# Optimization experiments

Measured on AMD Instinct MI355X. Metric: run time of the kernel, lower is better.

## Reference

```python
import jax, jax.numpy as jnp
import numpy as np

N, E, D = 100000, 1600000, 128      # nodes, edges, in_channels = MLP out_dim
L = 3                               # num GIN layers
OC = D + L * D                      # concat width = 512
CH, CHID = 4, 256                   # num ChannelMLPs, their hidden dim


def setup_inputs() -> dict:
    key = jax.random.key(0)
    ks = jax.random.split(key, 10)
    s = lambda fan_in: 1.0 / np.sqrt(fan_in)
    x = jax.random.normal(ks[0], (N, D), dtype=jnp.float32)
    edge_index = jax.random.randint(ks[1], (2, E), 0, N, dtype=jnp.int32)
    # conv MLPs: per layer 3 linear layers (in->hid, hid->hid, hid->out), all 128x128
    convW = jax.random.normal(ks[2], (L, 3, D, D), dtype=jnp.float32) * s(D)
    convB = jnp.zeros((L, 3, D), dtype=jnp.float32)
    # channel MLPs: 512 -> 256 -> 256 -> 1, ReLU after every layer (output_activation='relu')
    chanW1 = jax.random.normal(ks[3], (CH, OC, CHID), dtype=jnp.float32) * s(OC)
    chanB1 = jnp.zeros((CH, CHID), dtype=jnp.float32)
    chanW2 = jax.random.normal(ks[4], (CH, CHID, CHID), dtype=jnp.float32) * s(CHID)
    chanB2 = jnp.zeros((CH, CHID), dtype=jnp.float32)
    chanW3 = jax.random.normal(ks[5], (CH, CHID, 1), dtype=jnp.float32) * s(CHID)
    chanB3 = jnp.zeros((CH, 1), dtype=jnp.float32)
    return {"x": x, "edge_index": edge_index, "convW": convW, "convB": convB,
            "chanW1": chanW1, "chanB1": chanB1, "chanW2": chanW2, "chanB2": chanB2,
            "chanW3": chanW3, "chanB3": chanB3}


def reference(x, edge_index, convW, convB, chanW1, chanB1, chanW2, chanB2, chanW3, chanB3):
    src, dst = edge_index[0], edge_index[1]
    n = x.shape[0]
    feats = [x]                      # skip_first_features=False -> keep input
    h = x
    for l in range(L):
        # GINConv, eps=0: mlp((1+eps)*h + sum_{j in N(i)} h_j)
        agg = jax.ops.segment_sum(h[src], dst, num_segments=n)  # scatter-add at targets
        h = h + agg
        for k in range(3):           # MLP: Lin+ReLU x3 (2 hidden + relu output activation)
            h = jax.nn.relu(h @ convW[l, k] + convB[l, k])
        feats.append(h)
    xcat = jnp.concatenate(feats, axis=1)                       # [N, 512]
    # channel MLPs vectorized over the channel axis c
    h1 = jax.nn.relu(jnp.einsum('nd,cdh->cnh', xcat, chanW1) + chanB1[:, None, :])
    h2 = jax.nn.relu(jnp.einsum('cnh,chk->cnk', h1, chanW2) + chanB2[:, None, :])
    h3 = jax.nn.relu(jnp.einsum('cnh,cho->cno', h2, chanW3) + chanB3[:, None, :])
    return jnp.transpose(h3[..., 0])                            # [N, num_ChannelMLPs]
```

## Files before the change

kernel.cpp:

```cpp
#include <hip/hip_runtime.h>
#include <hip/hip_bf16.h>

#define D 128
#define NLAYER 3
#define NCH 4

typedef __attribute__((ext_vector_type(8))) short short8;
typedef __attribute__((ext_vector_type(4))) float f32x4;

__device__ __forceinline__ ushort f2bf(float f) {
    unsigned int u = __builtin_bit_cast(unsigned int, f);
    u += 0x7fffu + ((u >> 16) & 1u);
    return (ushort)(u >> 16);
}
__device__ __forceinline__ float bflo(unsigned int u) {
    return __builtin_bit_cast(float, u << 16);
}
__device__ __forceinline__ float bfhi(unsigned int u) {
    return __builtin_bit_cast(float, u & 0xffff0000u);
}

#define FILL_CHUNK 4096
__global__ __launch_bounds__(256) void hist_part_kernel(
    const int* __restrict__ dst, int* __restrict__ deg,
    int E, int nPer, int N)
{
    int cls = blockIdx.x & 7;
    int base = (blockIdx.x >> 3) * FILL_CHUNK;
    int lo = cls * nPer;
    int hi = lo + nPer; if (hi > N) hi = N;
    int end = base + FILL_CHUNK; if (end > E) end = E;
    for (int e = base + threadIdx.x; e < end; e += 256) {
        int d = dst[e];
        if (d >= lo && d < hi) atomicAdd(&deg[d], 1);
    }
}

__global__ __launch_bounds__(256) void blocksum_kernel(
    const int* __restrict__ deg, int* __restrict__ bsum, int n)
{
    int i = blockIdx.x * 256 + threadIdx.x;
    int v = (i < n) ? deg[i] : 0;
#pragma unroll
    for (int o = 1; o < 64; o <<= 1) v += __shfl_xor(v, o);
    __shared__ int s[4];
    if ((threadIdx.x & 63) == 0) s[threadIdx.x >> 6] = v;
    __syncthreads();
    if (threadIdx.x == 0) bsum[blockIdx.x] = s[0] + s[1] + s[2] + s[3];
}

__global__ __launch_bounds__(512) void scanblk_kernel(
    const int* __restrict__ bsum, int* __restrict__ boff, int nb,
    int* __restrict__ offs, int n, int E)
{
    __shared__ int sh[512];
    int t = threadIdx.x;
    sh[t] = (t < nb) ? bsum[t] : 0;
    __syncthreads();
    for (int d = 1; d < 512; d <<= 1) {
        int v = (t >= d) ? sh[t - d] : 0;
        __syncthreads();
        sh[t] += v;
        __syncthreads();
    }
    if (t < nb) boff[t] = (t == 0) ? 0 : sh[t - 1];
    if (t == 0) offs[n] = E;
}

__global__ __launch_bounds__(256) void blockscan_kernel(
    const int* __restrict__ deg, const int* __restrict__ boff,
    int* __restrict__ offs, int* __restrict__ cursor, int n)
{
    __shared__ int sh[256];
    int t = threadIdx.x;
    int i = blockIdx.x * 256 + t;
    int v = (i < n) ? deg[i] : 0;
    sh[t] = v;
    __syncthreads();
    for (int d = 1; d < 256; d <<= 1) {
        int u = (t >= d) ? sh[t - d] : 0;
        __syncthreads();
        sh[t] += u;
        __syncthreads();
    }
    if (i < n) {
        int ex = boff[blockIdx.x] + sh[t] - v;
        offs[i] = ex; cursor[i] = ex;
    }
}

__global__ __launch_bounds__(256) void fill_part_kernel(
    const int* __restrict__ src, const int* __restrict__ dst,
    int* __restrict__ cursor, int* __restrict__ csr,
    int E, int nPer, int N)
{
    int cls = blockIdx.x & 7;
    int base = (blockIdx.x >> 3) * FILL_CHUNK;
    int lo = cls * nPer;
    int hi = lo + nPer; if (hi > N) hi = N;
    int end = base + FILL_CHUNK; if (end > E) end = E;
    for (int e = base + threadIdx.x; e < end; e += 256) {
        int d = dst[e];
        int s = src[e];
        if (d >= lo && d < hi) {
            int p = atomicAdd(&cursor[d], 1);
            csr[p] = s;
        }
    }
}

__global__ __launch_bounds__(256) void cvtx_kernel(
    const float* __restrict__ x, ushort* __restrict__ xb, int total8)
{
    int i = blockIdx.x * 256 + threadIdx.x;
    if (i >= total8) return;
    const float* gp = x + (size_t)i * 8;
    float4 v0 = *(const float4*)gp;
    float4 v1 = *(const float4*)(gp + 4);
    short8 pk;
    pk[0] = (short)f2bf(v0.x); pk[1] = (short)f2bf(v0.y);
    pk[2] = (short)f2bf(v0.z); pk[3] = (short)f2bf(v0.w);
    pk[4] = (short)f2bf(v1.x); pk[5] = (short)f2bf(v1.y);
    pk[6] = (short)f2bf(v1.z); pk[7] = (short)f2bf(v1.w);
    *(short8*)(xb + (size_t)i * 8) = pk;
}

__global__ void cvtW_kernel(const float* __restrict__ W, ushort* __restrict__ Wt,
                            int K, int Ncols) {
    __shared__ float tile[32][33];
    int c = blockIdx.z;
    int k0 = blockIdx.x * 32, n0 = blockIdx.y * 32;
    const float* Wc = W + (size_t)c * K * Ncols;
    ushort* Wtc = Wt + (size_t)c * K * Ncols;
    int tx = threadIdx.x & 31, ty = threadIdx.x >> 5;
#pragma unroll
    for (int i = 0; i < 4; ++i) {
        int k = k0 + ty + i * 8;
        tile[ty + i * 8][tx] = Wc[(size_t)k * Ncols + n0 + tx];
    }
    __syncthreads();
#pragma unroll
    for (int i = 0; i < 4; ++i) {
        int n = n0 + ty + i * 8;
        Wtc[(size_t)n * K + k0 + tx] = f2bf(tile[tx][ty + i * 8]);
    }
}

__global__ __launch_bounds__(256) void agg_bf16(
    const ushort* __restrict__ h,
    const int* __restrict__ offs, const int* __restrict__ csr,
    ushort* __restrict__ outb, int n)
{
    int node = (blockIdx.x * 256 + threadIdx.x) >> 4;
    int l16 = threadIdx.x & 15;
    if (node >= n) return;
    uint4 u = *((const uint4*)(h + (size_t)node * 128) + l16);
    float a0 = bflo(u.x), a1 = bfhi(u.x);
    float a2 = bflo(u.y), a3 = bfhi(u.y);
    float a4 = bflo(u.z), a5 = bfhi(u.z);
    float a6 = bflo(u.w), a7 = bfhi(u.w);
    int b = offs[node], e = offs[node + 1];
    int j = b;
    for (; j + 4 <= e; j += 4) {
        int s0 = csr[j], s1 = csr[j + 1], s2 = csr[j + 2], s3 = csr[j + 3];
        uint4 v0 = *((const uint4*)(h + (size_t)s0 * 128) + l16);
        uint4 v1 = *((const uint4*)(h + (size_t)s1 * 128) + l16);
        uint4 v2 = *((const uint4*)(h + (size_t)s2 * 128) + l16);
        uint4 v3 = *((const uint4*)(h + (size_t)s3 * 128) + l16);
        a0 += (bflo(v0.x) + bflo(v1.x)) + (bflo(v2.x) + bflo(v3.x));
        a1 += (bfhi(v0.x) + bfhi(v1.x)) + (bfhi(v2.x) + bfhi(v3.x));
        a2 += (bflo(v0.y) + bflo(v1.y)) + (bflo(v2.y) + bflo(v3.y));
        a3 += (bfhi(v0.y) + bfhi(v1.y)) + (bfhi(v2.y) + bfhi(v3.y));
        a4 += (bflo(v0.z) + bflo(v1.z)) + (bflo(v2.z) + bflo(v3.z));
        a5 += (bfhi(v0.z) + bfhi(v1.z)) + (bfhi(v2.z) + bfhi(v3.z));
        a6 += (bflo(v0.w) + bflo(v1.w)) + (bflo(v2.w) + bflo(v3.w));
        a7 += (bfhi(v0.w) + bfhi(v1.w)) + (bfhi(v2.w) + bfhi(v3.w));
    }
    for (; j < e; ++j) {
        uint4 v0 = *((const uint4*)(h + (size_t)csr[j] * 128) + l16);
        a0 += bflo(v0.x); a1 += bfhi(v0.x);
        a2 += bflo(v0.y); a3 += bfhi(v0.y);
        a4 += bflo(v0.z); a5 += bfhi(v0.z);
        a6 += bflo(v0.w); a7 += bfhi(v0.w);
    }
    uint4 po;
    po.x = (unsigned int)f2bf(a0) | ((unsigned int)f2bf(a1) << 16);
    po.y = (unsigned int)f2bf(a2) | ((unsigned int)f2bf(a3) << 16);
    po.z = (unsigned int)f2bf(a4) | ((unsigned int)f2bf(a5) << 16);
    po.w = (unsigned int)f2bf(a6) | ((unsigned int)f2bf(a7) << 16);
    *((uint4*)(outb + (size_t)node * 128) + l16) = po;
}

__global__ __launch_bounds__(256) void gin_mlp_mfma(
    const ushort* __restrict__ A,
    const ushort* __restrict__ WtL,
    const float* __restrict__ biasL,
    ushort* __restrict__ Out,
    int nrows)
{
    __shared__ __align__(16) ushort As[128 * 128];
    __shared__ __align__(16) ushort Bs[128 * 128];
    const int t = threadIdx.x;
    const int w = t >> 6, lane = t & 63;
    const int quad = lane >> 4, c15 = lane & 15;
    const int wr = w >> 1, wc = w & 1;
    const int rowbase = blockIdx.x * 128;

#pragma unroll
    for (int i = 0; i < 8; ++i) {
        int lin = (i * 4 + w) * 64 + lane;
        int row = lin >> 4, slot = lin & 15, g = slot ^ (row & 15);
        int grow = rowbase + row;
        if (grow >= nrows) grow = 0;
        const ushort* gp = A + (size_t)grow * 128 + g * 8;
        __builtin_amdgcn_global_load_lds(
            (const __attribute__((address_space(1))) void*)gp,
            (__attribute__((address_space(3))) void*)&As[(i * 4 + w) * 512],
            16, 0, 0);
    }
#pragma unroll
    for (int i = 0; i < 8; ++i) {
        int lin = (i * 4 + w) * 64 + lane;
        int n = lin >> 4, slot = lin & 15, g = slot ^ (n & 15);
        const ushort* gp = WtL + (size_t)n * 128 + g * 8;
        __builtin_amdgcn_global_load_lds(
            (const __attribute__((address_space(1))) void*)gp,
            (__attribute__((address_space(3))) void*)&Bs[(i * 4 + w) * 512],
            16, 0, 0);
    }
    __syncthreads();

    for (int s = 0; s < 3; ++s) {
        f32x4 acc[4][4];
#pragma unroll
        for (int i = 0; i < 4; ++i)
#pragma unroll
            for (int j = 0; j < 4; ++j)
#pragma unroll
                for (int r = 0; r < 4; ++r) acc[i][j][r] = 0.f;

#pragma unroll
        for (int ks = 0; ks < 4; ++ks) {
            short8 af[4], bf[4];
#pragma unroll
            for (int tr = 0; tr < 4; ++tr) {
                int r = wr * 64 + tr * 16 + c15;
                af[tr] = *(const short8*)&As[r * 128 + (((ks * 4 + quad) ^ (r & 15)) * 8)];
            }
#pragma unroll
            for (int tc = 0; tc < 4; ++tc) {
                int n = wc * 64 + tc * 16 + c15;
                bf[tc] = *(const short8*)&Bs[n * 128 + (((ks * 4 + quad) ^ (n & 15)) * 8)];
            }
#pragma unroll
            for (int tr = 0; tr < 4; ++tr)
#pragma unroll
                for (int tc = 0; tc < 4; ++tc)
                    acc[tr][tc] = __builtin_amdgcn_mfma_f32_16x16x32_bf16(
                        af[tr], bf[tc], acc[tr][tc], 0, 0, 0);
        }
        __syncthreads();

        if (s < 2) {
#pragma unroll
            for (int tc = 0; tc < 4; ++tc) {
                int col = wc * 64 + tc * 16 + c15;
                float bv = biasL[s * 128 + col];
#pragma unroll
                for (int tr = 0; tr < 4; ++tr)
#pragma unroll
                    for (int rg = 0; rg < 4; ++rg) {
                        int row = wr * 64 + tr * 16 + quad * 4 + rg;
                        As[row * 128 + (((col >> 3) ^ (row & 15)) * 8) + (col & 7)]
                            = f2bf(fmaxf(acc[tr][tc][rg] + bv, 0.f));
                    }
            }
            const ushort* Wn = WtL + (size_t)(s + 1) * 128 * 128;
#pragma unroll
            for (int i = 0; i < 8; ++i) {
                int lin = (i * 4 + w) * 64 + lane;
                int n = lin >> 4, slot = lin & 15, g = slot ^ (n & 15);
                const ushort* gp = Wn + (size_t)n * 128 + g * 8;
                __builtin_amdgcn_global_load_lds(
                    (const __attribute__((address_space(1))) void*)gp,
                    (__attribute__((address_space(3))) void*)&Bs[(i * 4 + w) * 512],
                    16, 0, 0);
            }
            __syncthreads();
        } else {
#pragma unroll
            for (int tc = 0; tc < 4; ++tc) {
                int col = wc * 64 + tc * 16 + c15;
                float bv = biasL[2 * 128 + col];
#pragma unroll
                for (int tr = 0; tr < 4; ++tr)
#pragma unroll
                    for (int rg = 0; rg < 4; ++rg) {
                        int grow = rowbase + wr * 64 + tr * 16 + quad * 4 + rg;
                        if (grow < nrows)
                            Out[(size_t)grow * 128 + col]
                                = f2bf(fmaxf(acc[tr][tc][rg] + bv, 0.f));
                    }
            }
        }
    }
}

__global__ __launch_bounds__(256, 2) void chan_fused_mfma(
    const ushort* __restrict__ A0, const ushort* __restrict__ A1,
    const ushort* __restrict__ A2, const ushort* __restrict__ A3,
    const ushort* __restrict__ Wt1,
    const float* __restrict__ b1,
    const ushort* __restrict__ Wt2,
    const float* __restrict__ b2,
    const float* __restrict__ w3,
    const float* __restrict__ b3,
    float* __restrict__ out,
    int N, int T, int chunkT)
{
    const int bid = blockIdx.x;
    const int xcd = bid & 7;
    const int idx = bid >> 3;
    const int c = idx & 3;
    const int rt = xcd * chunkT + (idx >> 2);
    if (rt >= T) return;
    const int rowbase = rt * 64;

    __shared__ __align__(16) ushort As2[2][64 * 32];
    __shared__ __align__(16) ushort Bs2[2][256 * 32];
    __shared__ __align__(16) ushort Ts[64 * 256];
    __shared__ float red[64][4];
    const int t = threadIdx.x;
    const int w = t >> 6, lane = t & 63;
    const int quad = lane >> 4, c15 = lane & 15;
    const ushort* W1c = Wt1 + (size_t)c * 256 * 512;
    const ushort* W2c = Wt2 + (size_t)c * 256 * 256;

    const int a_lin = w * 64 + lane;
    const int a_row = a_lin >> 2, a_slot = a_lin & 3;
    const int a_g = a_slot ^ ((a_row >> 1) & 3);
    int a_grow = rowbase + a_row; if (a_grow >= N) a_grow = 0;
    int b_n[4], b_g[4];
#pragma unroll
    for (int i = 0; i < 4; ++i) {
        int lin = (i * 4 + w) * 64 + lane;
        b_n[i] = lin >> 2;
        b_g[i] = (lin & 3) ^ ((b_n[i] >> 1) & 3);
    }

    auto stageA = [&](int buf, int kc) {
        int ai = kc >> 7;
        const ushort* Ab = (ai == 0) ? A0 : (ai == 1) ? A1 : (ai == 2) ? A2 : A3;
        const ushort* gp = Ab + (size_t)a_grow * 128 + (kc & 127) + a_g * 8;
        __builtin_amdgcn_global_load_lds(
            (const __attribute__((address_space(1))) void*)gp,
            (__attribute__((address_space(3))) void*)&As2[buf][w * 512],
            16, 0, 0);
    };
    auto stageB = [&](int buf, const ushort* Wn, int ldk, int kc) {
#pragma unroll
        for (int i = 0; i < 4; ++i) {
            const ushort* gp = Wn + (size_t)b_n[i] * ldk + kc + b_g[i] * 8;
            __builtin_amdgcn_global_load_lds(
                (const __attribute__((address_space(1))) void*)gp,
                (__attribute__((address_space(3))) void*)&Bs2[buf][(i * 4 + w) * 512],
                16, 0, 0);
        }
    };

    f32x4 acc[4][4];
#pragma unroll
    for (int i = 0; i < 4; ++i)
#pragma unroll
        for (int j = 0; j < 4; ++j)
#pragma unroll
            for (int r = 0; r < 4; ++r) acc[i][j][r] = 0.f;

    stageA(0, 0);
    stageB(0, W1c, 512, 0);
    __syncthreads();
#pragma unroll 2
    for (int s = 0; s < 16; ++s) {
        const int cur = s & 1, nxt = cur ^ 1;
        if (s < 15) {
            stageA(nxt, (s + 1) * 32);
            stageB(nxt, W1c, 512, (s + 1) * 32);
        } else {
            stageB(nxt, W2c, 256, 0);
        }
        short8 af[4], bf[4];
#pragma unroll
        for (int tr = 0; tr < 4; ++tr) {
            int r = tr * 16 + c15;
            af[tr] = *(const short8*)&As2[cur][r * 32 + ((quad ^ ((r >> 1) & 3)) * 8)];
        }
#pragma unroll
        for (int tc = 0; tc < 4; ++tc) {
            int n = w * 64 + tc * 16 + c15;
            bf[tc] = *(const short8*)&Bs2[cur][n * 32 + ((quad ^ ((n >> 1) & 3)) * 8)];
        }
#pragma unroll
        for (int tr = 0; tr < 4; ++tr)
#pragma unroll
            for (int tc = 0; tc < 4; ++tc)
                acc[tr][tc] = __builtin_amdgcn_mfma_f32_16x16x32_bf16(
                    af[tr], bf[tc], acc[tr][tc], 0, 0, 0);
        __syncthreads();
    }

#pragma unroll
    for (int tc = 0; tc < 4; ++tc) {
        int col = w * 64 + tc * 16 + c15;
        float bv = b1[c * 256 + col];
#pragma unroll
        for (int tr = 0; tr < 4; ++tr)
#pragma unroll
            for (int rg = 0; rg < 4; ++rg) {
                int row = tr * 16 + quad * 4 + rg;
                Ts[row * 256 + (((col >> 3) ^ (row & 31)) * 8) + (col & 7)]
                    = f2bf(fmaxf(acc[tr][tc][rg] + bv, 0.f));
            }
    }
    __syncthreads();

#pragma unroll
    for (int i = 0; i < 4; ++i)
#pragma unroll
        for (int j = 0; j < 4; ++j)
#pragma unroll
            for (int r = 0; r < 4; ++r) acc[i][j][r] = 0.f;

#pragma unroll 2
    for (int s = 0; s < 8; ++s) {
        const int cur = s & 1, nxt = cur ^ 1;
        if (s < 7) stageB(nxt, W2c, 256, (s + 1) * 32);
        short8 af[4], bf[4];
        const int g0 = s * 4 + quad;
#pragma unroll
        for (int tr = 0; tr < 4; ++tr) {
            int r = tr * 16 + c15;
            af[tr] = *(const short8*)&Ts[r * 256 + ((g0 ^ (r & 31)) * 8)];
        }
#pragma unroll
        for (int tc = 0; tc < 4; ++tc) {
            int n = w * 64 + tc * 16 + c15;
            bf[tc] = *(const short8*)&Bs2[cur][n * 32 + ((quad ^ ((n >> 1) & 3)) * 8)];
        }
#pragma unroll
        for (int tr = 0; tr < 4; ++tr)
#pragma unroll
            for (int tc = 0; tc < 4; ++tc)
                acc[tr][tc] = __builtin_amdgcn_mfma_f32_16x16x32_bf16(
                    af[tr], bf[tc], acc[tr][tc], 0, 0, 0);
        __syncthreads();
    }

    float b2v[4], w3v[4];
#pragma unroll
    for (int tc = 0; tc < 4; ++tc) {
        int col = w * 64 + tc * 16 + c15;
        b2v[tc] = b2[c * 256 + col];
        w3v[tc] = w3[c * 256 + col];
    }
#pragma unroll
    for (int tr = 0; tr < 4; ++tr)
#pragma unroll
        for (int rg = 0; rg < 4; ++rg) {
            float p = 0.f;
#pragma unroll
            for (int tc = 0; tc < 4; ++tc)
                p += fmaxf(acc[tr][tc][rg] + b2v[tc], 0.f) * w3v[tc];
            p += __shfl_xor(p, 1);
            p += __shfl_xor(p, 2);
            p += __shfl_xor(p, 4);
            p += __shfl_xor(p, 8);
            if (c15 == 0) red[tr * 16 + quad * 4 + rg][w] = p;
        }
    __syncthreads();
    if (t < 64) {
        int grow = rowbase + t;
        if (grow < N) {
            float s = red[t][0] + red[t][1] + red[t][2] + red[t][3] + b3[c];
            out[(size_t)grow * NCH + c] = fmaxf(s, 0.f);
        }
    }
}

extern "C" void kernel_launch(void* const* d_in, const int* in_sizes, int n_in,
                              void* d_out, int out_size, void* d_ws, size_t ws_size,
                              hipStream_t stream) {
    const float* x        = (const float*)d_in[0];
    const int*   eidx     = (const int*)d_in[1];
    const float* convW    = (const float*)d_in[2];
    const float* convB    = (const float*)d_in[3];
    const float* chanW1   = (const float*)d_in[4];
    const float* chanB1   = (const float*)d_in[5];
    const float* chanW2   = (const float*)d_in[6];
    const float* chanB2   = (const float*)d_in[7];
    const float* chanW3   = (const float*)d_in[8];
    const float* chanB3   = (const float*)d_in[9];
    float* out = (float*)d_out;

    const int N = in_sizes[0] / D;
    const int E = in_sizes[1] / 2;
    const int* srcp = eidx;
    const int* dstp = eidx + E;
    const int nb = (N + 255) / 256;

    char* w = (char*)d_ws;
    auto take = [&](size_t bytes) {
        char* p = w;
        w += (bytes + 255) & ~(size_t)255;
        return p;
    };
    ushort* xb     = (ushort*)take((size_t)N * D * 2);
    ushort* h0     = (ushort*)take((size_t)N * D * 2);
    ushort* h1     = (ushort*)take((size_t)N * D * 2);
    ushort* h2     = (ushort*)take((size_t)N * D * 2);
    int*    deg    = (int*)take((size_t)N * 4);
    int*    offs   = (int*)take((size_t)(N + 1) * 4);
    int*    cursor = (int*)take((size_t)N * 4);
    int*    bsum   = (int*)take((size_t)nb * 4);
    int*    boff   = (int*)take((size_t)nb * 4);
    ushort* Wt1b   = (ushort*)take((size_t)NCH * 256 * 512 * 2);
    ushort* Wt2b   = (ushort*)take((size_t)NCH * 256 * 256 * 2);
    ushort* WtC    = (ushort*)take((size_t)NLAYER * 3 * D * D * 2);

    size_t used = (size_t)(w - (char*)d_ws);
    if (used > ws_size) return;
    size_t rem = ws_size - used;
    size_t need_gin = (((size_t)E * 4 + 255) & ~(size_t)255) + (size_t)N * D * 2;
    if (rem < need_gin) return;

    int*    csr = (int*)w;
    ushort* a   = (ushort*)(w + (((size_t)E * 4 + 255) & ~(size_t)255));

    hipMemsetAsync(deg, 0, (size_t)N * 4, stream);
    {
        int nchunks = (E + FILL_CHUNK - 1) / FILL_CHUNK;
        int nPer = (N + 7) / 8;
        hist_part_kernel<<<nchunks * 8, 256, 0, stream>>>(dstp, deg, E, nPer, N);
        blocksum_kernel<<<nb, 256, 0, stream>>>(deg, bsum, N);
        scanblk_kernel<<<1, 512, 0, stream>>>(bsum, boff, nb, offs, N, E);
        blockscan_kernel<<<nb, 256, 0, stream>>>(deg, boff, offs, cursor, N);
        fill_part_kernel<<<nchunks * 8, 256, 0, stream>>>(
            srcp, dstp, cursor, csr, E, nPer, N);
    }

    cvtx_kernel<<<(N * 16 + 255) / 256, 256, 0, stream>>>(x, xb, N * 16);
    cvtW_kernel<<<dim3(512 / 32, 256 / 32, NCH), 256, 0, stream>>>(chanW1, Wt1b, 512, 256);
    cvtW_kernel<<<dim3(256 / 32, 256 / 32, NCH), 256, 0, stream>>>(chanW2, Wt2b, 256, 256);
    cvtW_kernel<<<dim3(D / 32, D / 32, NLAYER * 3), 256, 0, stream>>>(convW, WtC, D, D);

    const int rowtiles = (N + 127) / 128;
    const int aggblocks = (N * 16 + 255) / 256;

    ushort* hbuf[NLAYER] = {h0, h1, h2};
    const ushort* prev = xb;
    for (int l = 0; l < NLAYER; ++l) {
        agg_bf16<<<aggblocks, 256, 0, stream>>>(prev, offs, csr, a, N);
        gin_mlp_mfma<<<rowtiles, 256, 0, stream>>>(
            a, WtC + (size_t)l * 3 * D * D, convB + (size_t)l * 3 * D, hbuf[l], N);
        prev = hbuf[l];
    }

    {
        const int T = (N + 63) / 64;
        const int chunkT = (T + 7) / 8;
        const int grid = 8 * chunkT * NCH;
        chan_fused_mfma<<<grid, 256, 0, stream>>>(
            xb, h0, h1, h2,
            Wt1b, chanB1, Wt2b, chanB2, chanW3, chanB3,
            out, N, T, chunkT);
    }
}
```

Before: 885.6 us.

## Load channel-MLP A tiles to registers, widen K-step, alias hidden tile onto B buffer

The first channel-MLP GEMM now loads A-operand fragments straight from global memory into registers, double-buffered in registers, instead of staging them through LDS. Both GEMMs now use a 64-wide K step with an XOR swizzle over 8 groups. The hidden-activation tile Ts now shares storage with the second B buffer, which cuts LDS use. The cost is that the second GEMM loses double buffering: each W2 chunk is loaded between two barriers, so memory latency is exposed there.

After: 925.0 us. 4.5% more time.

```diff
diff --git a/kernel.cpp b/kernel.cpp
--- a/kernel.cpp
+++ b/kernel.cpp
@@ -326,40 +326,26 @@
     if (rt >= T) return;
     const int rowbase = rt * 64;
 
-    __shared__ __align__(16) ushort As2[2][64 * 32];
-    __shared__ __align__(16) ushort Bs2[2][256 * 32];
-    __shared__ __align__(16) ushort Ts[64 * 256];
+    __shared__ __align__(16) ushort Bs2[2][256 * 64];
     __shared__ float red[64][4];
+    ushort* Ts = &Bs2[1][0];
+
     const int t = threadIdx.x;
     const int w = t >> 6, lane = t & 63;
     const int quad = lane >> 4, c15 = lane & 15;
     const ushort* W1c = Wt1 + (size_t)c * 256 * 512;
     const ushort* W2c = Wt2 + (size_t)c * 256 * 256;
 
-    const int a_lin = w * 64 + lane;
-    const int a_row = a_lin >> 2, a_slot = a_lin & 3;
-    const int a_g = a_slot ^ ((a_row >> 1) & 3);
-    int a_grow = rowbase + a_row; if (a_grow >= N) a_grow = 0;
-    int b_n[4], b_g[4];
-#pragma unroll
-    for (int i = 0; i < 4; ++i) {
+    int b_n[8], b_g[8];
+#pragma unroll
+    for (int i = 0; i < 8; ++i) {
         int lin = (i * 4 + w) * 64 + lane;
-        b_n[i] = lin >> 2;
-        b_g[i] = (lin & 3) ^ ((b_n[i] >> 1) & 3);
-    }
-
-    auto stageA = [&](int buf, int kc) {
-        int ai = kc >> 7;
-        const ushort* Ab = (ai == 0) ? A0 : (ai == 1) ? A1 : (ai == 2) ? A2 : A3;
-        const ushort* gp = Ab + (size_t)a_grow * 128 + (kc & 127) + a_g * 8;
-        __builtin_amdgcn_global_load_lds(
-            (const __attribute__((address_space(1))) void*)gp,
-            (__attribute__((address_space(3))) void*)&As2[buf][w * 512],
-            16, 0, 0);
-    };
+        b_n[i] = lin >> 3;
+        b_g[i] = (lin & 7) ^ (b_n[i] & 7);
+    }
     auto stageB = [&](int buf, const ushort* Wn, int ldk, int kc) {
 #pragma unroll
-        for (int i = 0; i < 4; ++i) {
+        for (int i = 0; i < 8; ++i) {
             const ushort* gp = Wn + (size_t)b_n[i] * ldk + kc + b_g[i] * 8;
             __builtin_amdgcn_global_load_lds(
                 (const __attribute__((address_space(1))) void*)gp,
@@ -368,6 +354,24 @@
         }
     };
 
+    int growv[4];
+#pragma unroll
+    for (int tr = 0; tr < 4; ++tr) {
+        int g = rowbase + tr * 16 + c15;
+        growv[tr] = (g < N) ? g : 0;
+    }
+    auto loadA = [&](short8 (&dst)[4][2], int kc) {
+        int ai = kc >> 7;
+        const ushort* Ab = (ai == 0) ? A0 : (ai == 1) ? A1 : (ai == 2) ? A2 : A3;
+        const int within = kc & 127;
+#pragma unroll
+        for (int tr = 0; tr < 4; ++tr) {
+            const ushort* rp = Ab + (size_t)growv[tr] * 128 + within + quad * 8;
+            dst[tr][0] = *(const short8*)(rp);
+            dst[tr][1] = *(const short8*)(rp + 32);
+        }
+    };
+
     f32x4 acc[4][4];
 #pragma unroll
     for (int i = 0; i < 4; ++i)
@@ -376,35 +380,34 @@
 #pragma unroll
             for (int r = 0; r < 4; ++r) acc[i][j][r] = 0.f;
 
-    stageA(0, 0);
+    short8 afb[2][4][2];
+    loadA(afb[0], 0);
     stageB(0, W1c, 512, 0);
     __syncthreads();
-#pragma unroll 2
-    for (int s = 0; s < 16; ++s) {
+#pragma unroll
+    for (int s = 0; s < 8; ++s) {
         const int cur = s & 1, nxt = cur ^ 1;
-        if (s < 15) {
-            stageA(nxt, (s + 1) * 32);
-            stageB(nxt, W1c, 512, (s + 1) * 32);
+        if (s < 7) {
+            loadA(afb[nxt], (s + 1) * 64);
+            stageB(nxt, W1c, 512, (s + 1) * 64);
         } else {
-            stageB(nxt, W2c, 256, 0);
-        }
-        short8 af[4], bf[4];
-#pragma unroll
-        for (int tr = 0; tr < 4; ++tr) {
-            int r = tr * 16 + c15;
-            af[tr] = *(const short8*)&As2[cur][r * 32 + ((quad ^ ((r >> 1) & 3)) * 8)];
-        }
-#pragma unroll
-        for (int tc = 0; tc < 4; ++tc) {
-            int n = w * 64 + tc * 16 + c15;
-            bf[tc] = *(const short8*)&Bs2[cur][n * 32 + ((quad ^ ((n >> 1) & 3)) * 8)];
-        }
-#pragma unroll
-        for (int tr = 0; tr < 4; ++tr)
-#pragma unroll
-            for (int tc = 0; tc < 4; ++tc)
-                acc[tr][tc] = __builtin_amdgcn_mfma_f32_16x16x32_bf16(
-                    af[tr], bf[tc], acc[tr][tc], 0, 0, 0);
+            stageB(0, W2c, 256, 0);
+        }
+#pragma unroll
+        for (int ks = 0; ks < 2; ++ks) {
+            short8 bf[4];
+#pragma unroll
+            for (int tc = 0; tc < 4; ++tc) {
+                int n = w * 64 + tc * 16 + c15;
+                bf[tc] = *(const short8*)&Bs2[cur][n * 64 + (((ks * 4 + quad) ^ (n & 7)) * 8)];
+            }
+#pragma unroll
+            for (int tr = 0; tr < 4; ++tr)
+#pragma unroll
+                for (int tc = 0; tc < 4; ++tc)
+                    acc[tr][tc] = __builtin_amdgcn_mfma_f32_16x16x32_bf16(
+                        afb[cur][tr][ks], bf[tc], acc[tr][tc], 0, 0, 0);
+        }
         __syncthreads();
     }
 
@@ -430,29 +433,34 @@
 #pragma unroll
             for (int r = 0; r < 4; ++r) acc[i][j][r] = 0.f;
 
-#pragma unroll 2
-    for (int s = 0; s < 8; ++s) {
-        const int cur = s & 1, nxt = cur ^ 1;
-        if (s < 7) stageB(nxt, W2c, 256, (s + 1) * 32);
-        short8 af[4], bf[4];
-        const int g0 = s * 4 + quad;
-#pragma unroll
-        for (int tr = 0; tr < 4; ++tr) {
-            int r = tr * 16 + c15;
-            af[tr] = *(const short8*)&Ts[r * 256 + ((g0 ^ (r & 31)) * 8)];
-        }
-#pragma unroll
-        for (int tc = 0; tc < 4; ++tc) {
-            int n = w * 64 + tc * 16 + c15;
-            bf[tc] = *(const short8*)&Bs2[cur][n * 32 + ((quad ^ ((n >> 1) & 3)) * 8)];
-        }
-#pragma unroll
-        for (int tr = 0; tr < 4; ++tr)
-#pragma unroll
-            for (int tc = 0; tc < 4; ++tc)
-                acc[tr][tc] = __builtin_amdgcn_mfma_f32_16x16x32_bf16(
-                    af[tr], bf[tc], acc[tr][tc], 0, 0, 0);
-        __syncthreads();
+#pragma unroll
+    for (int s = 0; s < 4; ++s) {
+#pragma unroll
+        for (int ks = 0; ks < 2; ++ks) {
+            short8 af[4], bf[4];
+            const int g0 = s * 8 + ks * 4 + quad;
+#pragma unroll
+            for (int tr = 0; tr < 4; ++tr) {
+                int r = tr * 16 + c15;
+                af[tr] = *(const short8*)&Ts[r * 256 + ((g0 ^ (r & 31)) * 8)];
+            }
+#pragma unroll
+            for (int tc = 0; tc < 4; ++tc) {
+                int n = w * 64 + tc * 16 + c15;
+                bf[tc] = *(const short8*)&Bs2[0][n * 64 + (((ks * 4 + quad) ^ (n & 7)) * 8)];
+            }
+#pragma unroll
+            for (int tr = 0; tr < 4; ++tr)
+#pragma unroll
+                for (int tc = 0; tc < 4; ++tc)
+                    acc[tr][tc] = __builtin_amdgcn_mfma_f32_16x16x32_bf16(
+                        af[tr], bf[tc], acc[tr][tc], 0, 0, 0);
+        }
+        if (s < 3) {
+            __syncthreads();
+            stageB(0, W2c, 256, (s + 1) * 64);
+            __syncthreads();
+        }
     }
 
     float b2v[4], w3v[4];
```
